# Optimization experiments

Measured on AMD Instinct MI355X. Metric: run time of the kernel, lower is better.

## Reference

```python
import jax, jax.numpy as jnp
import numpy as np

D = 768
H = 12
HD = D // H
NQ = 100
KV = 257
SEQ = NQ + KV
BS = 32


def layer_norm(x, g, b):
    # torch LayerNorm computed in fp32 then cast back (LayerNorm subclass)
    xf = x.astype(jnp.float32)
    m = xf.mean(-1, keepdims=True)
    v = ((xf - m) ** 2).mean(-1, keepdims=True)
    return ((xf - m) / jnp.sqrt(v + 1e-5) * g + b).astype(x.dtype)


def setup_inputs() -> dict:
    key = jax.random.key(0)
    ks = jax.random.split(key, 8)
    s = 0.02
    return {
        "y": jax.random.normal(ks[0], (SEQ, BS, D), jnp.float32),
        "attn_mask": jax.random.bernoulli(ks[1], 0.3, (BS, NQ, KV)),
        "in_proj_w": jax.random.normal(ks[2], (3 * D, D), jnp.float32) * s,
        "in_proj_b": jnp.zeros((3 * D,), jnp.float32),
        "new_q_w": jax.random.normal(ks[3], (D, D), jnp.float32) * s,
        "new_q_b": jnp.zeros((D,), jnp.float32),
        "out_w": jax.random.normal(ks[4], (D, D), jnp.float32) * s,
        "out_b": jnp.zeros((D,), jnp.float32),
        "ln1_g": jnp.ones((D,), jnp.float32),
        "ln1_b": jnp.zeros((D,), jnp.float32),
        "ln2_g": jnp.ones((D,), jnp.float32),
        "ln2_b": jnp.zeros((D,), jnp.float32),
        "fc_w": jax.random.normal(ks[5], (4 * D, D), jnp.float32) * s,
        "fc_b": jnp.zeros((4 * D,), jnp.float32),
        "proj_w": jax.random.normal(ks[6], (D, 4 * D), jnp.float32) * s,
        "proj_b": jnp.zeros((D,), jnp.float32),
    }


def _attention(x, attn_mask, in_proj_w, in_proj_b, new_q_w, new_q_b, out_w, out_b):
    # x: [seq, bs, D] (already ln_1'd); attn_mask: [bs, nq, kv] bool
    seq, bs, d = x.shape
    nq = attn_mask.shape[1]
    scale = 1.0 / np.sqrt(HD)
    # k/v (and the clip queries) come from the detached non-query tokens
    xkv = jax.lax.stop_gradient(x[nq:])  # [kv, bs, D]
    qkv = xkv @ in_proj_w.T + in_proj_b
    q, k, v = jnp.split(qkv, 3, axis=-1)

    def heads(t):  # [S, bs, D] -> [bs, H, S, hd]
        return t.reshape(t.shape[0], bs, H, HD).transpose(1, 2, 0, 3)

    q = heads(q) * scale
    k = heads(k)
    v = heads(v)
    # regular (clip) attention over shared k/v
    clip_attn = jnp.einsum('bhld,bhmd->bhlm', q, k)
    clip_out = jnp.einsum('bhlm,bhmd->bhld', jax.nn.softmax(clip_attn, axis=-1), v)
    # mask-conditioned queries via new_q_proj (NOT detached)
    new_q = heads(x[:nq] @ new_q_w.T + new_q_b) * scale  # [bs, H, nq, hd]
    bias = jnp.where(attn_mask[:, None], -jnp.inf, 0.0).astype(q.dtype)  # [bs,1,nq,kv]
    mask_attn = jnp.einsum('bhqd,bhmd->bhqm', new_q, k) + bias
    mask_out = jnp.einsum('bhqm,bhmd->bhqd', jax.nn.softmax(mask_attn, axis=-1), v)

    def merge(t):  # [bs, H, S, hd] -> [S, bs, D]
        return t.transpose(2, 0, 1, 3).reshape(t.shape[2], bs, d)

    attn_out = jnp.concatenate([merge(mask_out), merge(clip_out)], axis=0)
    return attn_out @ out_w.T + out_b


def reference(y, attn_mask, in_proj_w, in_proj_b, new_q_w, new_q_b, out_w, out_b,
              ln1_g, ln1_b, ln2_g, ln2_b, fc_w, fc_b, proj_w, proj_b):
    x = layer_norm(y, ln1_g, ln1_b)
    y = y + _attention(x, attn_mask, in_proj_w, in_proj_b, new_q_w, new_q_b, out_w, out_b)
    h = layer_norm(y, ln2_g, ln2_b)
    h = h @ fc_w.T + fc_b
    h = h * jax.nn.sigmoid(1.702 * h)  # QuickGELU
    return y + (h @ proj_w.T + proj_b)
```

## Files before the change

### kernel.cpp

```cpp
#include <hip/hip_runtime.h>


typedef short bf16x8 __attribute__((ext_vector_type(8)));
typedef float f32x4 __attribute__((ext_vector_type(4)));
typedef unsigned short u16;
typedef unsigned long long u64;

__device__ __forceinline__ u16 f2b(float f) {
    unsigned u = __builtin_bit_cast(unsigned, f);
    u = (u + 0x7fffu + ((u >> 16) & 1u)) >> 16;
    return (u16)u;
}
__device__ __forceinline__ float b2f(u16 h) {
    unsigned u = ((unsigned)h) << 16;
    return __builtin_bit_cast(float, u);
}
__device__ __forceinline__ unsigned pack2(float a, float b) {
    return (unsigned)f2b(a) | ((unsigned)f2b(b) << 16);
}
__device__ __forceinline__ void g2l16(const void* g, void* l) {
    __builtin_amdgcn_global_load_lds(
        (__attribute__((address_space(1))) void*)g,
        (__attribute__((address_space(3))) void*)l, 16, 0, 0);
}
#define MFMA16(a, b, c) __builtin_amdgcn_mfma_f32_16x16x32_bf16((a), (b), (c), 0, 0, 0)

__global__ __launch_bounds__(256) void cvt5_kernel(
    const float* __restrict__ s0, const float* __restrict__ s1, const float* __restrict__ s2,
    const float* __restrict__ s3, const float* __restrict__ s4, u16* __restrict__ dst)
{
    int i = blockIdx.x * 256 + threadIdx.x;
    int stride = gridDim.x * 256;
    for (; i < 1916928; i += stride) {
        const float* src; int off;
        if (i < 442368)       { src = s0; off = i; }
        else if (i < 589824)  { src = s1; off = i - 442368; }
        else if (i < 737280)  { src = s2; off = i - 589824; }
        else if (i < 1327104) { src = s3; off = i - 737280; }
        else                  { src = s4; off = i - 1327104; }
        float4 v = ((const float4*)src)[off];
        ushort4 o;
        o.x = f2b(v.x); o.y = f2b(v.y); o.z = f2b(v.z); o.w = f2b(v.w);
        ((ushort4*)dst)[i] = o;
    }
}

__global__ __launch_bounds__(256) void mask_pack(const int* __restrict__ m, u64* __restrict__ o) {
    int row = blockIdx.x * 4 + (threadIdx.x >> 6);
    int lane = threadIdx.x & 63;
    if (row >= 3200) return;
    const int* r = m + (size_t)row * 257;
    u64 w0 = __ballot(r[lane] != 0);
    u64 w1 = __ballot(r[64 + lane] != 0);
    u64 w2 = __ballot(r[128 + lane] != 0);
    u64 w3 = __ballot(r[192 + lane] != 0);
    u64 w4 = __ballot(lane == 0 && r[256] != 0);
    if (lane == 0) {
        u64* p = o + (size_t)row * 5;
        p[0] = w0; p[1] = w1; p[2] = w2; p[3] = w3; p[4] = w4;
    }
}

__global__ __launch_bounds__(256) void ln_kernel(
    const float* __restrict__ in, const float* __restrict__ g, const float* __restrict__ be,
    u16* __restrict__ out, int nrows)
{
    int row = blockIdx.x * 4 + (threadIdx.x >> 6);
    int lane = threadIdx.x & 63;
    if (row >= nrows) return;
    const float* p = in + (size_t)row * 768;
    float4 a0 = *(const float4*)(p + lane * 4);
    float4 a1 = *(const float4*)(p + 256 + lane * 4);
    float4 a2 = *(const float4*)(p + 512 + lane * 4);
    float s = a0.x + a0.y + a0.z + a0.w + a1.x + a1.y + a1.z + a1.w + a2.x + a2.y + a2.z + a2.w;
    for (int o = 32; o; o >>= 1) s += __shfl_xor(s, o);
    float mean = s * (1.f / 768.f);
    float vs = 0.f;
#define SQA(t) { float dx; dx = t.x-mean; vs += dx*dx; dx = t.y-mean; vs += dx*dx; dx = t.z-mean; vs += dx*dx; dx = t.w-mean; vs += dx*dx; }
    SQA(a0) SQA(a1) SQA(a2)
#undef SQA
    for (int o = 32; o; o >>= 1) vs += __shfl_xor(vs, o);
    float rstd = rsqrtf(vs * (1.f / 768.f) + 1e-5f);
    u16* orow = out + (size_t)row * 768;
#pragma unroll
    for (int i = 0; i < 3; ++i) {
        int d = i * 256 + lane * 4;
        float4 av = (i == 0) ? a0 : ((i == 1) ? a1 : a2);
        float4 gv = *(const float4*)(g + d);
        float4 bv = *(const float4*)(be + d);
        ushort4 ov;
        ov.x = f2b((av.x - mean) * rstd * gv.x + bv.x);
        ov.y = f2b((av.y - mean) * rstd * gv.y + bv.y);
        ov.z = f2b((av.z - mean) * rstd * gv.z + bv.z);
        ov.w = f2b((av.w - mean) * rstd * gv.w + bv.w);
        *(ushort4*)(orow + d) = ov;
    }
}

template<int ACT, int OUTBF, int RES>
__global__ __launch_bounds__(256) void gemm_bt(
    const u16* __restrict__ A, const u16* __restrict__ B,
    const float* __restrict__ bias, const float* __restrict__ res,
    void* __restrict__ Cp, int M, int N, int K)
{
    __shared__ u16 Al[2][128 * 32];
    __shared__ u16 Bl[2][128 * 32];
    const int t = threadIdx.x;
    const int lane = t & 63, w = t >> 6;
    const int wr = w >> 1, wc = w & 1;
    const int fr = lane & 15, fg = lane >> 4;

    const int raw = blockIdx.x + gridDim.x * blockIdx.y;
    const int rows_per = gridDim.x >> 3;
    const int gy = gridDim.y;
    const int xcd = raw & 7, idx = raw >> 3;
    const int nt = idx % gy;
    const int mt = xcd * rows_per + idx / gy;
    const int m0 = mt * 128, n0 = nt * 128;
    if (m0 >= M) return;

    const int srow = lane >> 2;
    const int scol = (lane & 3) * 8;
    int ar0 = m0 + w * 32 + srow;      int ar1 = ar0 + 16;
    ar0 = ar0 < M ? ar0 : M - 1;       ar1 = ar1 < M ? ar1 : M - 1;
    int br0 = n0 + w * 32 + srow;      int br1 = br0 + 16;
    br0 = br0 < N ? br0 : N - 1;       br1 = br1 < N ? br1 : N - 1;
    const u16* a0p = A + (size_t)ar0 * K + scol;
    const u16* a1p = A + (size_t)ar1 * K + scol;
    const u16* b0p = B + (size_t)br0 * K + scol;
    const u16* b1p = B + (size_t)br1 * K + scol;
    const int lo0 = (w * 2 + 0) * 512, lo1 = (w * 2 + 1) * 512;

    const int nk = K >> 5;
    g2l16(a0p, &Al[0][lo0]);
    g2l16(a1p, &Al[0][lo1]);
    g2l16(b0p, &Bl[0][lo0]);
    g2l16(b1p, &Bl[0][lo1]);
    __syncthreads();

    f32x4 acc[4][4] = {};
#pragma unroll 2
    for (int ki = 0; ki < nk; ++ki) {
        const int cur = ki & 1;
        if (ki + 1 < nk) {
            const int k0 = (ki + 1) << 5;
            const int nxt = cur ^ 1;
            g2l16(a0p + k0, &Al[nxt][lo0]);
            g2l16(a1p + k0, &Al[nxt][lo1]);
            g2l16(b0p + k0, &Bl[nxt][lo0]);
            g2l16(b1p + k0, &Bl[nxt][lo1]);
        }
        bf16x8 af[4], bfr[4];
#pragma unroll
        for (int m = 0; m < 4; ++m) af[m] = *(const bf16x8*)&Al[cur][(wr * 64 + m * 16 + fr) * 32 + fg * 8];
#pragma unroll
        for (int n = 0; n < 4; ++n) bfr[n] = *(const bf16x8*)&Bl[cur][(wc * 64 + n * 16 + fr) * 32 + fg * 8];
#pragma unroll
        for (int m = 0; m < 4; ++m)
#pragma unroll
            for (int n = 0; n < 4; ++n)
                acc[m][n] = MFMA16(af[m], bfr[n], acc[m][n]);
        __syncthreads();
    }
#pragma unroll
    for (int m = 0; m < 4; ++m) {
#pragma unroll
        for (int n = 0; n < 4; ++n) {
            int col = n0 + wc * 64 + n * 16 + fr;
            float bv = bias[col];
#pragma unroll
            for (int r = 0; r < 4; ++r) {
                int row = m0 + wr * 64 + m * 16 + fg * 4 + r;
                if (row < M) {
                    float v = acc[m][n][r] + bv;
                    if (RES) v += res[(size_t)row * N + col];
                    if (ACT) v = v / (1.f + __expf(-1.702f * v));
                    if (OUTBF) ((u16*)Cp)[(size_t)row * N + col] = f2b(v);
                    else       ((float*)Cp)[(size_t)row * N + col] = v;
                }
            }
        }
    }
}

__global__ __launch_bounds__(512) void attn_kernel(
    const u16* __restrict__ qkv,
    const u16* __restrict__ nq,
    const u64* __restrict__ mpk,
    u16* __restrict__ out)
{
    __shared__ u16 Kl[264 * 64];
    __shared__ u16 Vt[64 * 296];
    __shared__ u16 Pb[8][640];
    const int raw = blockIdx.x;
    const int bid = (raw & 7) * 48 + (raw >> 3);
    const int b = bid / 12, h = bid % 12;
    const int t = threadIdx.x, lane = t & 63, wv = t >> 6;
    const int fr = lane & 15, fg = lane >> 4;

    for (int i = t; i < 2048; i += 512) {
        int d = i >> 5, c = 257 + (i & 31);
        if (c < 288) Vt[d * 296 + c] = 0;
    }
    {
        const int r8 = t >> 3, c8 = (t & 7) * 8;
        const u16* kb = qkv + 768 + h * 64 + c8;
        const u16* vb = qkv + 1536 + h * 64 + c8;
#pragma unroll 1
        for (int p = 0; p < 5; ++p) {
            int m = r8 + p * 64;
            if (m <= 256) {
                size_t go = (size_t)(m * 32 + b) * 2304;
                bf16x8 kv = *(const bf16x8*)(kb + go);
                int byte = m * 128 + c8 * 2;
                *(bf16x8*)((char*)Kl + (byte ^ ((m & 7) << 4))) = kv;
                bf16x8 vv = *(const bf16x8*)(vb + go);
#pragma unroll
                for (int j = 0; j < 8; ++j)
                    Vt[(c8 + j) * 296 + m] = (u16)vv[j];
            }
        }
    }
    __syncthreads();

    const int swzK = (fr & 7) << 4;
    char* pb = (char*)&Pb[wv][0];
    const char* KlB = (const char*)Kl;
    const char* VtB = (const char*)Vt;

    auto fetch = [&](int ti, bf16x8& q0v, bf16x8& q1v, u64* mw, bool& im) {
        int q = ti * 16 + fr;
        int qc = q < 357 ? q : 356;
        im = qc < 100;
        const u16* qp = im ? (nq + (size_t)(qc * 32 + b) * 768 + h * 64)
                           : (qkv + (size_t)((qc - 100) * 32 + b) * 2304 + h * 64);
        q0v = *(const bf16x8*)(qp + fg * 8);
        q1v = *(const bf16x8*)(qp + 32 + fg * 8);
        if (im) {
            const u64* mp = mpk + (size_t)(b * 100 + qc) * 5;
            mw[0] = mp[0]; mw[1] = mp[1]; mw[2] = mp[2]; mw[3] = mp[3]; mw[4] = mp[4];
        } else {
            mw[0] = mw[1] = mw[2] = mw[3] = mw[4] = 0;
        }
    };

    bf16x8 qf0, qf1, qn0, qn1;
    u64 mwc[5], mwn[5];
    bool imc, imn;
    fetch(wv, qf0, qf1, mwc, imc);

#pragma unroll 1
    for (int ti = wv; ti < 23; ti += 8) {
        f32x4 sc[17];
#pragma unroll
        for (int kt = 0; kt < 17; ++kt) {
            int rb = (kt * 16 + fr) * 128;
            bf16x8 ka0 = *(const bf16x8*)(KlB + ((rb + fg * 16) ^ swzK));
            bf16x8 ka1 = *(const bf16x8*)(KlB + ((rb + 64 + fg * 16) ^ swzK));
            f32x4 a = {0.f, 0.f, 0.f, 0.f};
            a = MFMA16(ka0, qf0, a);
            a = MFMA16(ka1, qf1, a);
            sc[kt] = a;
        }
        if (ti + 8 < 23) fetch(ti + 8, qn0, qn1, mwn, imn);
        float mx = -INFINITY;
#pragma unroll
        for (int kt = 0; kt < 17; ++kt) {
            u64 mw = (kt >> 2) == 0 ? mwc[0] : (kt >> 2) == 1 ? mwc[1] : (kt >> 2) == 2 ? mwc[2]
                   : (kt >> 2) == 3 ? mwc[3] : mwc[4];
#pragma unroll
            for (int r = 0; r < 4; ++r) {
                int key = kt * 16 + fg * 4 + r;
                bool bad = (key > 256) || (imc && ((mw >> (key & 63)) & 1ull));
                float s = bad ? -INFINITY : sc[kt][r];
                sc[kt][r] = s;
                mx = fmaxf(mx, s);
            }
        }
        mx = fmaxf(mx, __shfl_xor(mx, 16));
        mx = fmaxf(mx, __shfl_xor(mx, 32));
        float l = 0.f;
        unsigned pk[17][2];
#pragma unroll
        for (int kt = 0; kt < 17; ++kt) {
            float p0 = __expf((sc[kt][0] - mx) * 0.125f);
            float p1 = __expf((sc[kt][1] - mx) * 0.125f);
            float p2 = __expf((sc[kt][2] - mx) * 0.125f);
            float p3 = __expf((sc[kt][3] - mx) * 0.125f);
            l += (p0 + p1) + (p2 + p3);
            pk[kt][0] = pack2(p0, p1);
            pk[kt][1] = pack2(p2, p3);
        }
        l += __shfl_xor(l, 16);
        l += __shfl_xor(l, 32);
        f32x4 oc[4] = {};
#pragma unroll
        for (int c = 0; c < 9; ++c) {
            uint2 w0; w0.x = pk[2 * c][0]; w0.y = pk[2 * c][1];
            *(uint2*)(pb + fr * 80 + fg * 8) = w0;
            uint2 w1;
            if (c < 8) { w1.x = pk[2 * c + 1][0]; w1.y = pk[2 * c + 1][1]; }
            else       { w1.x = 0; w1.y = 0; }
            *(uint2*)(pb + fr * 80 + 32 + fg * 8) = w1;
            bf16x8 pf = *(const bf16x8*)(pb + fr * 80 + fg * 16);
#pragma unroll
            for (int dt = 0; dt < 4; ++dt) {
                bf16x8 vf = *(const bf16x8*)(VtB + (dt * 16 + fr) * 592 + c * 64 + fg * 16);
                oc[dt] = MFMA16(vf, pf, oc[dt]);
            }
        }
        int q = ti * 16 + fr;
        if (q < 357) {
            float rl = 1.f / l;
            u16* op = out + (size_t)(q * 32 + b) * 768 + h * 64 + fg * 4;
#pragma unroll
            for (int dt = 0; dt < 4; ++dt) {
                ushort4 ov;
                ov.x = f2b(oc[dt][0] * rl); ov.y = f2b(oc[dt][1] * rl);
                ov.z = f2b(oc[dt][2] * rl); ov.w = f2b(oc[dt][3] * rl);
                *(ushort4*)(op + dt * 16) = ov;
            }
        }
        if (ti + 8 < 23) {
            qf0 = qn0; qf1 = qn1; imc = imn;
            mwc[0] = mwn[0]; mwc[1] = mwn[1]; mwc[2] = mwn[2]; mwc[3] = mwn[3]; mwc[4] = mwn[4];
        }
    }
}

extern "C" void kernel_launch(void* const* d_in, const int* in_sizes, int n_in,
                              void* d_out, int out_size, void* d_ws, size_t ws_size,
                              hipStream_t stream)
{
    const float* y   = (const float*)d_in[0];
    const int*   msk = (const int*)  d_in[1];
    const float* ipw = (const float*)d_in[2];
    const float* ipb = (const float*)d_in[3];
    const float* nqw = (const float*)d_in[4];
    const float* nqb = (const float*)d_in[5];
    const float* ow  = (const float*)d_in[6];
    const float* ob  = (const float*)d_in[7];
    const float* l1g = (const float*)d_in[8];
    const float* l1b = (const float*)d_in[9];
    const float* l2g = (const float*)d_in[10];
    const float* l2b = (const float*)d_in[11];
    const float* fcw = (const float*)d_in[12];
    const float* fcb = (const float*)d_in[13];
    const float* pjw = (const float*)d_in[14];
    const float* pjb = (const float*)d_in[15];

    char* ws = (char*)d_ws;
    u16* x_b   = (u16*)(ws + 0);
    u16* qkv_b = (u16*)(ws + 17547264);
    u16* nq_b  = (u16*)(ws + 55443456);
    u16* ao_b  = (u16*)(ws + 60358656);
    u16* h1_b  = (u16*)(ws + 0);
    u16* h_b   = (u16*)(ws + 77905920);
    u64* mpk_b = (u64*)(ws + 77905920);
    u16* w_ip  = (u16*)(ws + 95453184);
    float* out = (float*)d_out;

    cvt5_kernel<<<2048, 256, 0, stream>>>(ipw, nqw, ow, fcw, pjw, w_ip);
    mask_pack<<<800, 256, 0, stream>>>(msk, mpk_b);

    u16* w_nq  = w_ip + 1769472;
    u16* w_out = w_nq + 589824;
    u16* w_fc  = w_out + 589824;
    u16* w_pj  = w_fc + 2359296;

    ln_kernel<<<2856, 256, 0, stream>>>(y, l1g, l1b, x_b, 11424);
    gemm_bt<0, 1, 0><<<dim3(72, 18), 256, 0, stream>>>(x_b + (size_t)3200 * 768, w_ip, ipb, nullptr, qkv_b, 8224, 2304, 768);
    gemm_bt<0, 1, 0><<<dim3(32, 6), 256, 0, stream>>>(x_b, w_nq, nqb, nullptr, nq_b, 3200, 768, 768);
    attn_kernel<<<384, 512, 0, stream>>>(qkv_b, nq_b, mpk_b, ao_b);
    gemm_bt<0, 0, 1><<<dim3(96, 6), 256, 0, stream>>>(ao_b, w_out, ob, y, out, 11424, 768, 768);
    ln_kernel<<<2856, 256, 0, stream>>>(out, l2g, l2b, h_b, 11424);
    gemm_bt<1, 1, 0><<<dim3(96, 24), 256, 0, stream>>>(h_b, w_fc, fcb, nullptr, h1_b, 11424, 3072, 768);
    gemm_bt<0, 0, 1><<<dim3(96, 6), 256, 0, stream>>>(h1_b, w_pj, pjb, out, out, 11424, 768, 3072);
}
```

Before: 459.9 us.

## Pre-transpose K/V per head into contiguous layout and stage attention output

Adds a kv_transpose kernel that writes each (batch, head) K block (swizzled) and V-transposed block contiguously, so the attention kernel can fill LDS with direct global-to-LDS copies instead of strided loads and scalar transposed LDS stores. Attention output is written to a contiguous per-head buffer and scattered back to the token-major layout by a separate o_untranspose kernel. This trades two extra launches and extra global traffic for cheaper LDS staging and coalesced output writes in the attention kernel.

```diff
diff --git a/kernel.cpp b/kernel.cpp
--- a/kernel.cpp
+++ b/kernel.cpp
@@ -183,14 +183,82 @@
     }
 }
 
+__global__ __launch_bounds__(256) void kv_transpose(
+    const u16* __restrict__ qkv, u16* __restrict__ kvq)
+{
+    __shared__ u16 vl[64][80];
+    const int bh = blockIdx.x;
+    const int b = bh / 12, h = bh % 12;
+    const int t = threadIdx.x;
+    char* dstK = (char*)kvq + (size_t)bh * 71680;
+    u16*  dstV = kvq + (size_t)bh * 35840 + 16896;
+    const u16* kb = qkv + 768 + h * 64;
+    const u16* vb = qkv + 1536 + h * 64;
+
+    {
+        const int r = t >> 3, c8 = (t & 7) * 8;
+#pragma unroll 1
+        for (int p = 0; p < 9; ++p) {
+            int m = r + p * 32;
+            if (m < 264) {
+                bf16x8 k8 = {0, 0, 0, 0, 0, 0, 0, 0};
+                if (m <= 256) k8 = *(const bf16x8*)(kb + (size_t)(m * 32 + b) * 2304 + c8);
+                *(bf16x8*)(dstK + m * 128 + ((c8 * 2) ^ ((m & 7) << 4))) = k8;
+            }
+        }
+    }
+#pragma unroll 1
+    for (int m0 = 0; m0 < 320; m0 += 64) {
+        {
+            const int r = t >> 3, c8 = (t & 7) * 8;
+#pragma unroll
+            for (int p = 0; p < 2; ++p) {
+                int mm = r + p * 32, m = m0 + mm;
+                bf16x8 v8 = {0, 0, 0, 0, 0, 0, 0, 0};
+                if (m <= 256) v8 = *(const bf16x8*)(vb + (size_t)(m * 32 + b) * 2304 + c8);
+                *(bf16x8*)&vl[mm][c8] = v8;
+            }
+        }
+        __syncthreads();
+        {
+            const int d = t >> 2;
+#pragma unroll
+            for (int p = 0; p < 2; ++p) {
+                int mloc = ((t & 3) + p * 4) * 8;
+                int col = m0 + mloc;
+                if (col < 296) {
+                    bf16x8 o8;
+#pragma unroll
+                    for (int j = 0; j < 8; ++j) o8[j] = (short)vl[mloc + j][d];
+                    *(bf16x8*)(dstV + d * 296 + col) = o8;
+                }
+            }
+        }
+        __syncthreads();
+    }
+}
+
+__global__ __launch_bounds__(256) void o_untranspose(
+    const u16* __restrict__ ot, u16* __restrict__ ao)
+{
+    int idx = blockIdx.x * 256 + threadIdx.x;
+    if (idx >= 384 * 357 * 8) return;
+    int bh = idx / (357 * 8);
+    int rem = idx - bh * (357 * 8);
+    int q = rem >> 3, g = rem & 7;
+    int b = bh / 12, h = bh % 12;
+    bf16x8 v = *(const bf16x8*)(ot + (size_t)idx * 8);
+    *(bf16x8*)(ao + (size_t)(q * 32 + b) * 768 + h * 64 + g * 8) = v;
+}
+
 __global__ __launch_bounds__(512) void attn_kernel(
+    const u16* __restrict__ kvq,
     const u16* __restrict__ qkv,
     const u16* __restrict__ nq,
     const u64* __restrict__ mpk,
-    u16* __restrict__ out)
-{
-    __shared__ u16 Kl[264 * 64];
-    __shared__ u16 Vt[64 * 296];
+    u16* __restrict__ ot)
+{
+    __shared__ u16 KV[35840];
     __shared__ u16 Pb[8][640];
     const int raw = blockIdx.x;
     const int bid = (raw & 7) * 48 + (raw >> 3);
@@ -198,35 +266,21 @@
     const int t = threadIdx.x, lane = t & 63, wv = t >> 6;
     const int fr = lane & 15, fg = lane >> 4;
 
-    for (int i = t; i < 2048; i += 512) {
-        int d = i >> 5, c = 257 + (i & 31);
-        if (c < 288) Vt[d * 296 + c] = 0;
-    }
     {
-        const int r8 = t >> 3, c8 = (t & 7) * 8;
-        const u16* kb = qkv + 768 + h * 64 + c8;
-        const u16* vb = qkv + 1536 + h * 64 + c8;
-#pragma unroll 1
-        for (int p = 0; p < 5; ++p) {
-            int m = r8 + p * 64;
-            if (m <= 256) {
-                size_t go = (size_t)(m * 32 + b) * 2304;
-                bf16x8 kv = *(const bf16x8*)(kb + go);
-                int byte = m * 128 + c8 * 2;
-                *(bf16x8*)((char*)Kl + (byte ^ ((m & 7) << 4))) = kv;
-                bf16x8 vv = *(const bf16x8*)(vb + go);
-#pragma unroll
-                for (int j = 0; j < 8; ++j)
-                    Vt[(c8 + j) * 296 + m] = (u16)vv[j];
-            }
+        const char* src = (const char*)kvq + (size_t)bid * 71680;
+        char* dst = (char*)KV;
+#pragma unroll
+        for (int i = 0; i < 9; ++i) {
+            int g = wv * 9 + i;
+            if (g < 70) g2l16(src + g * 1024 + lane * 16, dst + g * 1024);
         }
     }
     __syncthreads();
 
     const int swzK = (fr & 7) << 4;
     char* pb = (char*)&Pb[wv][0];
-    const char* KlB = (const char*)Kl;
-    const char* VtB = (const char*)Vt;
+    const char* KlB = (const char*)KV;
+    const char* VtB = (const char*)KV + 33792;
 
     auto fetch = [&](int ti, bf16x8& q0v, bf16x8& q1v, u64* mw, bool& im) {
         int q = ti * 16 + fr;
@@ -312,7 +366,7 @@
         int q = ti * 16 + fr;
         if (q < 357) {
             float rl = 1.f / l;
-            u16* op = out + (size_t)(q * 32 + b) * 768 + h * 64 + fg * 4;
+            u16* op = ot + ((size_t)bid * 357 + q) * 64 + fg * 4;
 #pragma unroll
             for (int dt = 0; dt < 4; ++dt) {
                 ushort4 ov;
@@ -354,9 +408,11 @@
     u16* qkv_b = (u16*)(ws + 17547264);
     u16* nq_b  = (u16*)(ws + 55443456);
     u16* ao_b  = (u16*)(ws + 60358656);
+    u16* kvq_t = (u16*)(ws + 60358656);
+    u16* o_t   = (u16*)(ws + 0);
     u16* h1_b  = (u16*)(ws + 0);
     u16* h_b   = (u16*)(ws + 77905920);
-    u64* mpk_b = (u64*)(ws + 77905920);
+    u64* mpk_b = (u64*)(ws + 87883776);
     u16* w_ip  = (u16*)(ws + 95453184);
     float* out = (float*)d_out;
 
@@ -371,7 +427,9 @@
     ln_kernel<<<2856, 256, 0, stream>>>(y, l1g, l1b, x_b, 11424);
     gemm_bt<0, 1, 0><<<dim3(72, 18), 256, 0, stream>>>(x_b + (size_t)3200 * 768, w_ip, ipb, nullptr, qkv_b, 8224, 2304, 768);
     gemm_bt<0, 1, 0><<<dim3(32, 6), 256, 0, stream>>>(x_b, w_nq, nqb, nullptr, nq_b, 3200, 768, 768);
-    attn_kernel<<<384, 512, 0, stream>>>(qkv_b, nq_b, mpk_b, ao_b);
+    kv_transpose<<<384, 256, 0, stream>>>(qkv_b, kvq_t);
+    attn_kernel<<<384, 512, 0, stream>>>(kvq_t, qkv_b, nq_b, mpk_b, o_t);
+    o_untranspose<<<4284, 256, 0, stream>>>(o_t, ao_b);
     gemm_bt<0, 0, 1><<<dim3(96, 6), 256, 0, stream>>>(ao_b, w_out, ob, y, out, 11424, 768, 768);
     ln_kernel<<<2856, 256, 0, stream>>>(out, l2g, l2b, h_b, 11424);
     gemm_bt<1, 1, 0><<<dim3(96, 24), 256, 0, stream>>>(h_b, w_fc, fcb, nullptr, h1_b, 11424, 3072, 768);
```

Result: slower. 480.4 us (+4.5%).
